# Performance work log

Hardware: AMD Instinct MI355X
Metric: run time of the kernel (lower is better)

Reference implementation:

```python
import jax, jax.numpy as jnp
import numpy as np

MARGIN = 1.0  # from init_kwargs


def _cdist(a, b):
    # Euclidean pairwise distances, [N, D] x [M, D] -> [N, M]
    sq = (jnp.sum(a * a, axis=1)[:, None]
          + jnp.sum(b * b, axis=1)[None, :]
          - 2.0 * (a @ b.T))
    return jnp.sqrt(jnp.maximum(sq, 0.0))


def setup_inputs() -> dict:
    key = jax.random.key(0)
    k1, k2 = jax.random.split(key)
    N, D = 8192, 128
    return {
        "output1": jax.random.normal(k1, (N, D), dtype=jnp.float32),
        "output2": jax.random.normal(k2, (N, D), dtype=jnp.float32),
    }


def reference(output1, output2):
    d = _cdist(output1, output2)  # [N, M]
    N, M = d.shape

    # image -> text direction (loop over rows i in the original)
    jmin = jnp.argmin(d, axis=1)            # [N] positive index per row
    pos_r = jnp.min(d, axis=1)              # [N] pos_distance = d[i, jmin[i]]
    hinge_r = jnp.maximum(0.0, MARGIN - pos_r[:, None] + d)  # [N, M]
    # exclude the positive (argmin) column from each row's mean
    hinge_r = jnp.where(jnp.arange(M)[None, :] == jmin[:, None], 0.0, hinge_r)
    image_losses = hinge_r.mean(axis=1)     # [N]

    # text -> image direction (loop over columns i in the original)
    imin = jnp.argmin(d, axis=0)            # [M]
    pos_c = jnp.min(d, axis=0)              # [M]
    hinge_c = jnp.maximum(0.0, MARGIN - pos_c[None, :] + d)  # [N, M]
    hinge_c = jnp.where(jnp.arange(N)[:, None] == imin[None, :], 0.0, hinge_c)
    text_losses = hinge_c.mean(axis=0)      # [M]

    return (image_losses.mean() + text_losses.mean()) * 0.5
```

## Files before the change

kernel.cpp:

```cpp
#include <hip/hip_runtime.h>
#include <hip/hip_bf16.h>
#include <math.h>

#define NN 8192
#define DD 128
#define BIGF 3.402823466e+38f

typedef __attribute__((ext_vector_type(8))) short short8;
typedef __attribute__((ext_vector_type(4))) float f32x4;

static __device__ __forceinline__ unsigned short bfc(float f) {
    return __bfloat16_as_ushort(__float2bfloat16(f));
}

__global__ __launch_bounds__(256) void prep_kernel(const float* __restrict__ A,
                                                   const float* __restrict__ B,
                                                   __hip_bfloat16* __restrict__ Abf,
                                                   __hip_bfloat16* __restrict__ Bbf,
                                                   float* __restrict__ na,
                                                   float* __restrict__ nb,
                                                   unsigned int* __restrict__ done) {
    if (blockIdx.y == 0 && blockIdx.x == 0 && threadIdx.x == 0) *done = 0u;
    const float* x = blockIdx.y ? B : A;
    __hip_bfloat16* xb = blockIdx.y ? Bbf : Abf;
    float* norm = blockIdx.y ? nb : na;
    const int sub = threadIdx.x >> 5;
    const int ch  = threadIdx.x & 31;
    const int row = blockIdx.x * 8 + sub;
    const float4 v = *(const float4*)(x + (size_t)row * DD + ch * 4);
    float s = v.x * v.x + v.y * v.y + v.z * v.z + v.w * v.w;
    uint2 pk;
    pk.x = ((unsigned)bfc(v.y) << 16) | bfc(v.x);
    pk.y = ((unsigned)bfc(v.w) << 16) | bfc(v.z);
    *(uint2*)(xb + (size_t)row * DD + ch * 4) = pk;
#pragma unroll
    for (int off = 16; off >= 1; off >>= 1) s += __shfl_xor(s, off, 64);
    if (ch == 0) norm[row] = s;
}

__global__ __launch_bounds__(256, 4) void dist_fused(
    const __hip_bfloat16* __restrict__ Ab, const __hip_bfloat16* __restrict__ Bb,
    const float* __restrict__ na, const float* __restrict__ nb,
    float* __restrict__ rowpart, float* __restrict__ colpart,
    float* __restrict__ totpart) {
    __shared__ char lds[32768];
    __shared__ float rmbuf[2][128];
    __shared__ float cmbuf[2][128];
    __shared__ float tbuf[4];
    char* ldsA = lds;
    char* ldsB = lds + 16384;
    const int tid = threadIdx.x;

    const int lin = blockIdx.y * 64 + blockIdx.x;
    const int swz = (lin & 7) * 512 + (lin >> 3);
    const int bx = swz & 63, by = swz >> 6;
    const int rowBase = by * 128;
    const int colBase = bx * 128;

    const unsigned short* aG = (const unsigned short*)Ab + (size_t)rowBase * DD;
    const unsigned short* bG = (const unsigned short*)Bb + (size_t)colBase * DD;

    const int l = tid & 63, wid = tid >> 6;
    const int wr = wid >> 1, wc = wid & 1;
    const int g = l >> 4, c = l & 15;

    f32x4 acc[4][4];
#pragma unroll
    for (int mi = 0; mi < 4; ++mi)
#pragma unroll
        for (int ni = 0; ni < 4; ++ni) acc[mi][ni] = (f32x4)0.f;

#pragma unroll
    for (int p = 0; p < 2; ++p) {
        if (p) __syncthreads();
#pragma unroll
        for (int it = 0; it < 4; ++it) {
            int idx = tid + 256 * it;
            int r = idx >> 3;
            int c16 = idx & 7;
            int dst = r * 128 + ((c16 * 16) ^ ((r & 7) << 4));
            *(short8*)(ldsA + dst) = *(const short8*)(aG + r * DD + p * 64 + c16 * 8);
            *(short8*)(ldsB + dst) = *(const short8*)(bG + r * DD + p * 64 + c16 * 8);
        }
        __syncthreads();
#pragma unroll
        for (int kk = 0; kk < 2; ++kk) {
            short8 af[4], bf[4];
            const int kbyte = kk * 64 + g * 16;
#pragma unroll
            for (int mi = 0; mi < 4; ++mi) {
                int r = wr * 64 + mi * 16 + c;
                af[mi] = *(const short8*)(ldsA + r * 128 + (kbyte ^ ((r & 7) << 4)));
                int r2 = wc * 64 + mi * 16 + c;
                bf[mi] = *(const short8*)(ldsB + r2 * 128 + (kbyte ^ ((r2 & 7) << 4)));
            }
#pragma unroll
            for (int mi = 0; mi < 4; ++mi)
#pragma unroll
                for (int ni = 0; ni < 4; ++ni)
                    acc[mi][ni] = __builtin_amdgcn_mfma_f32_16x16x32_bf16(
                        af[mi], bf[ni], acc[mi][ni], 0, 0, 0);
        }
    }

    const int row0 = rowBase + wr * 64;
    const int col0 = colBase + wc * 64;

    float nbc[4];
#pragma unroll
    for (int ni = 0; ni < 4; ++ni) nbc[ni] = nb[col0 + ni * 16 + c];

    float colm2[4] = {BIGF, BIGF, BIGF, BIGF};
    f32x4 tot4 = (f32x4)0.f;
#pragma unroll
    for (int mi = 0; mi < 4; ++mi) {
        const f32x4 na4 = *(const f32x4*)(na + row0 + mi * 16 + g * 4);
        float rowm2[4] = {BIGF, BIGF, BIGF, BIGF};
#pragma unroll
        for (int ni = 0; ni < 4; ++ni) {
            f32x4 a = acc[mi][ni];
#pragma unroll
            for (int reg = 0; reg < 4; ++reg) {
                float d2 = fmaf(-2.0f, a[reg], na4[reg] + nbc[ni]);
                rowm2[reg] = fminf(rowm2[reg], d2);
                colm2[ni] = fminf(colm2[ni], d2);
                tot4[reg] += __builtin_amdgcn_sqrtf(fmaxf(d2, 0.f));
            }
        }
#pragma unroll
        for (int reg = 0; reg < 4; ++reg) {
            float m = rowm2[reg];
            m = fminf(m, __shfl_xor(m, 1, 64));
            m = fminf(m, __shfl_xor(m, 2, 64));
            m = fminf(m, __shfl_xor(m, 4, 64));
            m = fminf(m, __shfl_xor(m, 8, 64));
            if (c == 0) rmbuf[wc][wr * 64 + mi * 16 + g * 4 + reg] = m;
        }
    }
#pragma unroll
    for (int ni = 0; ni < 4; ++ni) {
        float m = colm2[ni];
        m = fminf(m, __shfl_xor(m, 16, 64));
        m = fminf(m, __shfl_xor(m, 32, 64));
        if (g == 0) cmbuf[wr][wc * 64 + ni * 16 + c] = m;
    }
    float tot = (tot4[0] + tot4[1]) + (tot4[2] + tot4[3]);
#pragma unroll
    for (int off = 32; off >= 1; off >>= 1) tot += __shfl_xor(tot, off, 64);
    if (l == 0) tbuf[wid] = tot;
    __syncthreads();

    if (tid < 128) {
        rowpart[(size_t)bx * NN + rowBase + tid] = fminf(rmbuf[0][tid], rmbuf[1][tid]);
    } else if (tid < 256) {
        int j = tid - 128;
        colpart[(size_t)by * NN + colBase + j] = fminf(cmbuf[0][j], cmbuf[1][j]);
    }
    if (tid == 0)
        totpart[by * 64 + bx] = tbuf[0] + tbuf[1] + tbuf[2] + tbuf[3];
}

__global__ __launch_bounds__(256) void fin_kernel(const float* __restrict__ rowpart,
                                                  const float* __restrict__ colpart,
                                                  const float* __restrict__ totpart,
                                                  float* __restrict__ finpart,
                                                  unsigned int* __restrict__ done,
                                                  float* __restrict__ out) {
    const int idx = blockIdx.x * 256 + threadIdx.x;
    const int j = (idx < NN) ? idx : idx - NN;
    const float* p = (idx < NN) ? rowpart : colpart;
    float m = BIGF;
#pragma unroll 8
    for (int k = 0; k < 64; ++k) m = fminf(m, p[(size_t)k * NN + j]);
    float contrib = -__builtin_amdgcn_sqrtf(fmaxf(m, 0.f)) * (1.0f / 16384.0f);
    if (blockIdx.x < 16)
        contrib += totpart[blockIdx.x * 256 + threadIdx.x] * (1.0f / 67108864.0f);
#pragma unroll
    for (int off = 32; off >= 1; off >>= 1) contrib += __shfl_xor(contrib, off, 64);
    __shared__ float red[4];
    __shared__ unsigned last;
    if ((threadIdx.x & 63) == 0) red[threadIdx.x >> 6] = contrib;
    __syncthreads();
    if (threadIdx.x == 0) {
        finpart[blockIdx.x] = red[0] + red[1] + red[2] + red[3];
        __threadfence();
        last = (atomicAdd(done, 1u) == 63u) ? 1u : 0u;
    }
    __syncthreads();
    if (last && threadIdx.x < 64) {
        __threadfence();
        float s = __hip_atomic_load(&finpart[threadIdx.x], __ATOMIC_RELAXED,
                                    __HIP_MEMORY_SCOPE_AGENT);
#pragma unroll
        for (int off = 32; off >= 1; off >>= 1) s += __shfl_xor(s, off, 64);
        if (threadIdx.x == 0) out[0] = s + 1.0f - 1.0f / 8192.0f;
    }
}

extern "C" void kernel_launch(void* const* d_in, const int* in_sizes, int n_in,
                              void* d_out, int out_size, void* d_ws, size_t ws_size,
                              hipStream_t stream) {
    const float* A = (const float*)d_in[0];
    const float* B = (const float*)d_in[1];
    char* ws = (char*)d_ws;

    const size_t MB = 1024 * 1024;
    __hip_bfloat16* Abf = (__hip_bfloat16*)(ws);
    __hip_bfloat16* Bbf = (__hip_bfloat16*)(ws + 2 * MB);
    float* na      = (float*)(ws + 4 * MB);
    float* nb      = (float*)(ws + 4 * MB + 32768);
    float* rowpart = (float*)(ws + 4 * MB + 65536);
    float* colpart = (float*)(ws + 6 * MB + 65536);
    float* totpart = (float*)(ws + 8 * MB + 65536);
    float* finpart = (float*)(ws + 8 * MB + 65536 + 16384);
    unsigned int* done = (unsigned int*)(ws + 8 * MB + 65536 + 16384 + 256);

    dim3 pgrid(NN / 8, 2);
    prep_kernel<<<pgrid, 256, 0, stream>>>(A, B, Abf, Bbf, na, nb, done);

    dim3 grid(NN / 128, NN / 128);
    dist_fused<<<grid, 256, 0, stream>>>(Abf, Bbf, na, nb, rowpart, colpart, totpart);

    fin_kernel<<<64, 256, 0, stream>>>(rowpart, colpart, totpart, finpart, done,
                                       (float*)d_out);
}
```

Measured before the change: 66.72 us.

## Prefetch both K halves into registers and simplify final reduction with atomics

The GEMM tile loop now issues global loads for both K halves up front into registers. The second half's loads are in flight during the first half's MFMA phase, hiding global-memory latency instead of serialising load-then-compute twice. Launch bounds drop from 4 to 3 waves-per-EU to give room for the extra registers, at the cost of occupancy. The final reduction replaces the last-block counter pattern with a float atomicAdd into the output, which prep_kernel pre-initialises with the constant term. This makes the summation order nondeterministic.

```diff
diff --git a/kernel.cpp b/kernel.cpp
--- a/kernel.cpp
+++ b/kernel.cpp
@@ -19,8 +19,9 @@
                                                    __hip_bfloat16* __restrict__ Bbf,
                                                    float* __restrict__ na,
                                                    float* __restrict__ nb,
-                                                   unsigned int* __restrict__ done) {
-    if (blockIdx.y == 0 && blockIdx.x == 0 && threadIdx.x == 0) *done = 0u;
+                                                   float* __restrict__ out) {
+    if (blockIdx.x == 0 && blockIdx.y == 0 && threadIdx.x == 0)
+        out[0] = 1.0f - 1.0f / 8192.0f;
     const float* x = blockIdx.y ? B : A;
     __hip_bfloat16* xb = blockIdx.y ? Bbf : Abf;
     float* norm = blockIdx.y ? nb : na;
@@ -38,7 +39,7 @@
     if (ch == 0) norm[row] = s;
 }
 
-__global__ __launch_bounds__(256, 4) void dist_fused(
+__global__ __launch_bounds__(256, 3) void dist_fused(
     const __hip_bfloat16* __restrict__ Ab, const __hip_bfloat16* __restrict__ Bb,
     const float* __restrict__ na, const float* __restrict__ nb,
     float* __restrict__ rowpart, float* __restrict__ colpart,
@@ -50,6 +51,9 @@
     char* ldsA = lds;
     char* ldsB = lds + 16384;
     const int tid = threadIdx.x;
+    const int l = tid & 63, wid = tid >> 6;
+    const int wr = wid >> 1, wc = wid & 1;
+    const int g = l >> 4, c = l & 15;
 
     const int lin = blockIdx.y * 64 + blockIdx.x;
     const int swz = (lin & 7) * 512 + (lin >> 3);
@@ -60,9 +64,28 @@
     const unsigned short* aG = (const unsigned short*)Ab + (size_t)rowBase * DD;
     const unsigned short* bG = (const unsigned short*)Bb + (size_t)colBase * DD;
 
-    const int l = tid & 63, wid = tid >> 6;
-    const int wr = wid >> 1, wc = wid & 1;
-    const int g = l >> 4, c = l & 15;
+
+    short8 a0[4], b0[4], a1[4], b1[4];
+#pragma unroll
+    for (int it = 0; it < 4; ++it) {
+        int idx = tid + 256 * it, r = idx >> 3, c16 = idx & 7;
+        a0[it] = *(const short8*)(aG + r * DD + c16 * 8);
+        b0[it] = *(const short8*)(bG + r * DD + c16 * 8);
+    }
+#pragma unroll
+    for (int it = 0; it < 4; ++it) {
+        int idx = tid + 256 * it, r = idx >> 3, c16 = idx & 7;
+        a1[it] = *(const short8*)(aG + r * DD + 64 + c16 * 8);
+        b1[it] = *(const short8*)(bG + r * DD + 64 + c16 * 8);
+    }
+#pragma unroll
+    for (int it = 0; it < 4; ++it) {
+        int idx = tid + 256 * it, r = idx >> 3, c16 = idx & 7;
+        int dst = r * 128 + ((c16 * 16) ^ ((r & 7) << 4));
+        *(short8*)(ldsA + dst) = a0[it];
+        *(short8*)(ldsB + dst) = b0[it];
+    }
+    __syncthreads();
 
     f32x4 acc[4][4];
 #pragma unroll
@@ -70,38 +93,38 @@
 #pragma unroll
         for (int ni = 0; ni < 4; ++ni) acc[mi][ni] = (f32x4)0.f;
 
-#pragma unroll
-    for (int p = 0; p < 2; ++p) {
-        if (p) __syncthreads();
-#pragma unroll
-        for (int it = 0; it < 4; ++it) {
-            int idx = tid + 256 * it;
-            int r = idx >> 3;
-            int c16 = idx & 7;
-            int dst = r * 128 + ((c16 * 16) ^ ((r & 7) << 4));
-            *(short8*)(ldsA + dst) = *(const short8*)(aG + r * DD + p * 64 + c16 * 8);
-            *(short8*)(ldsB + dst) = *(const short8*)(bG + r * DD + p * 64 + c16 * 8);
-        }
-        __syncthreads();
-#pragma unroll
-        for (int kk = 0; kk < 2; ++kk) {
-            short8 af[4], bf[4];
-            const int kbyte = kk * 64 + g * 16;
-#pragma unroll
-            for (int mi = 0; mi < 4; ++mi) {
-                int r = wr * 64 + mi * 16 + c;
-                af[mi] = *(const short8*)(ldsA + r * 128 + (kbyte ^ ((r & 7) << 4)));
-                int r2 = wc * 64 + mi * 16 + c;
-                bf[mi] = *(const short8*)(ldsB + r2 * 128 + (kbyte ^ ((r2 & 7) << 4)));
-            }
-#pragma unroll
-            for (int mi = 0; mi < 4; ++mi)
-#pragma unroll
-                for (int ni = 0; ni < 4; ++ni)
-                    acc[mi][ni] = __builtin_amdgcn_mfma_f32_16x16x32_bf16(
-                        af[mi], bf[ni], acc[mi][ni], 0, 0, 0);
-        }
-    }
+#define COMPUTE_PHASE() do {                                                      \
+    _Pragma("unroll")                                                             \
+    for (int kk = 0; kk < 2; ++kk) {                                              \
+        short8 af[4], bf[4];                                                      \
+        const int kbyte = kk * 64 + g * 16;                                       \
+        _Pragma("unroll")                                                         \
+        for (int mi = 0; mi < 4; ++mi) {                                          \
+            int r = wr * 64 + mi * 16 + c;                                        \
+            af[mi] = *(const short8*)(ldsA + r * 128 + (kbyte ^ ((r & 7) << 4))); \
+            int r2 = wc * 64 + mi * 16 + c;                                       \
+            bf[mi] = *(const short8*)(ldsB + r2 * 128 + (kbyte ^ ((r2 & 7) << 4)));\
+        }                                                                         \
+        _Pragma("unroll")                                                         \
+        for (int mi = 0; mi < 4; ++mi)                                            \
+            _Pragma("unroll")                                                     \
+            for (int ni = 0; ni < 4; ++ni)                                        \
+                acc[mi][ni] = __builtin_amdgcn_mfma_f32_16x16x32_bf16(            \
+                    af[mi], bf[ni], acc[mi][ni], 0, 0, 0);                        \
+    } } while (0)
+
+    COMPUTE_PHASE();
+    __syncthreads();
+#pragma unroll
+    for (int it = 0; it < 4; ++it) {
+        int idx = tid + 256 * it, r = idx >> 3, c16 = idx & 7;
+        int dst = r * 128 + ((c16 * 16) ^ ((r & 7) << 4));
+        *(short8*)(ldsA + dst) = a1[it];
+        *(short8*)(ldsB + dst) = b1[it];
+    }
+    __syncthreads();
+    COMPUTE_PHASE();
+#undef COMPUTE_PHASE
 
     const int row0 = rowBase + wr * 64;
     const int col0 = colBase + wc * 64;
@@ -163,8 +186,6 @@
 __global__ __launch_bounds__(256) void fin_kernel(const float* __restrict__ rowpart,
                                                   const float* __restrict__ colpart,
                                                   const float* __restrict__ totpart,
-                                                  float* __restrict__ finpart,
-                                                  unsigned int* __restrict__ done,
                                                   float* __restrict__ out) {
     const int idx = blockIdx.x * 256 + threadIdx.x;
     const int j = (idx < NN) ? idx : idx - NN;
@@ -178,23 +199,10 @@
 #pragma unroll
     for (int off = 32; off >= 1; off >>= 1) contrib += __shfl_xor(contrib, off, 64);
     __shared__ float red[4];
-    __shared__ unsigned last;
     if ((threadIdx.x & 63) == 0) red[threadIdx.x >> 6] = contrib;
     __syncthreads();
-    if (threadIdx.x == 0) {
-        finpart[blockIdx.x] = red[0] + red[1] + red[2] + red[3];
-        __threadfence();
-        last = (atomicAdd(done, 1u) == 63u) ? 1u : 0u;
-    }
-    __syncthreads();
-    if (last && threadIdx.x < 64) {
-        __threadfence();
-        float s = __hip_atomic_load(&finpart[threadIdx.x], __ATOMIC_RELAXED,
-                                    __HIP_MEMORY_SCOPE_AGENT);
-#pragma unroll
-        for (int off = 32; off >= 1; off >>= 1) s += __shfl_xor(s, off, 64);
-        if (threadIdx.x == 0) out[0] = s + 1.0f - 1.0f / 8192.0f;
-    }
+    if (threadIdx.x == 0)
+        atomicAdd(out, red[0] + red[1] + red[2] + red[3]);
 }
 
 extern "C" void kernel_launch(void* const* d_in, const int* in_sizes, int n_in,
@@ -212,15 +220,12 @@
     float* rowpart = (float*)(ws + 4 * MB + 65536);
     float* colpart = (float*)(ws + 6 * MB + 65536);
     float* totpart = (float*)(ws + 8 * MB + 65536);
-    float* finpart = (float*)(ws + 8 * MB + 65536 + 16384);
-    unsigned int* done = (unsigned int*)(ws + 8 * MB + 65536 + 16384 + 256);
 
     dim3 pgrid(NN / 8, 2);
-    prep_kernel<<<pgrid, 256, 0, stream>>>(A, B, Abf, Bbf, na, nb, done);
+    prep_kernel<<<pgrid, 256, 0, stream>>>(A, B, Abf, Bbf, na, nb, (float*)d_out);
 
     dim3 grid(NN / 128, NN / 128);
     dist_fused<<<grid, 256, 0, stream>>>(Abf, Bbf, na, nb, rowpart, colpart, totpart);
 
-    fin_kernel<<<64, 256, 0, stream>>>(rowpart, colpart, totpart, finpart, done,
-                                       (float*)d_out);
-}
+    fin_kernel<<<64, 256, 0, stream>>>(rowpart, colpart, totpart, (float*)d_out);
+}
```

New measurement: 67.98 us. No clear change (+1.9%).
